# Performance work log

Hardware: AMD Instinct MI355X
Metric: run time of the kernel (lower is better)

The kernel has to match this reference:

```python
import jax, jax.numpy as jnp
import numpy as np

B = 131072
HIDDEN = 256


def setup_inputs() -> dict:
    key = jax.random.key(0)
    ks = jax.random.split(key, 9)
    x = jax.random.uniform(ks[0], (B, 2), dtype=jnp.float32)
    # torch nn.Linear weights are [out_features, in_features]; kaiming-uniform-ish scale
    def w(k, out_f, in_f):
        bound = 1.0 / np.sqrt(in_f)
        return jax.random.uniform(k, (out_f, in_f), jnp.float32, -bound, bound)
    W0 = w(ks[1], HIDDEN, 2)
    W1 = w(ks[2], HIDDEN, HIDDEN)
    W2 = w(ks[3], HIDDEN, HIDDEN)
    W3 = w(ks[4], HIDDEN, HIDDEN)
    W4 = w(ks[5], HIDDEN, HIDDEN)
    W5 = w(ks[6], HIDDEN, HIDDEN)
    W6 = w(ks[7], HIDDEN, HIDDEN)
    W7 = w(ks[8], 3, HIDDEN)
    return {"x": x, "W0": W0, "W1": W1, "W2": W2, "W3": W3,
            "W4": W4, "W5": W5, "W6": W6, "W7": W7}


def reference(x, W0, W1, W2, W3, W4, W5, W6, W7):
    # 8 bias-free Linear layers: ReLU after layers 0..6, Sigmoid after layer 7.
    h = x
    for W in (W0, W1, W2, W3, W4, W5, W6):
        h = jax.nn.relu(h @ W.T)
    return jax.nn.sigmoid(h @ W7.T)  # [B, 3]
```

## Files before the change

kernel.cpp:

```cpp
#include <hip/hip_runtime.h>
#include <hip/hip_bf16.h>


#define HID 256
#define BM 128
#define NBLK 1024
#define HPITCH 264

typedef __attribute__((ext_vector_type(8))) short bf16x8;
typedef __attribute__((ext_vector_type(8))) unsigned short u16x8;
typedef __attribute__((ext_vector_type(4))) unsigned short u16x4;
typedef __attribute__((ext_vector_type(4))) float f32x4;
typedef __attribute__((ext_vector_type(16))) float f32x16;

__device__ __forceinline__ unsigned cvt_pk_bf16(float lo, float hi) {
    unsigned r;
    asm("v_cvt_pk_bf16_f32 %0, %1, %2" : "=v"(r) : "v"(lo), "v"(hi));
    return r;
}

struct WPtrs { const float* w[6]; const float* w7; };

__global__ void pack_w_kernel(WPtrs wp, unsigned short* __restrict__ Wp) {
    int tid = blockIdx.x * 256 + threadIdx.x;
    if (tid < 49152) {
        int l  = tid & 63;
        int ft = (tid >> 6) & 1;
        int kk = (tid >> 7) & 15;
        int fw = (tid >> 11) & 3;
        int L  = tid >> 13;
        int n  = 64 * fw + 32 * ft + (l & 31);
        int k0 = 16 * kk + 8 * (l >> 5);
        const float* src = wp.w[L] + n * HID + k0;
        u16x8 v;
#pragma unroll
        for (int j = 0; j < 8; ++j) {
            union { float f; unsigned u; } c; c.f = src[j];
            unsigned r = c.u + 0x7fffu + ((c.u >> 16) & 1u);
            v[j] = (unsigned short)(r >> 16);
        }
        *(u16x8*)(Wp + (size_t)tid * 8) = v;
    } else if (tid < 49664) {
        int t  = tid - 49152;
        int l  = t & 63;
        int kk = t >> 6;
        int n  = l & 15;
        int k0 = 32 * kk + 8 * (l >> 4);
        u16x8 v;
#pragma unroll
        for (int j = 0; j < 8; ++j) {
            unsigned short s = 0;
            if (n < 3) {
                union { float f; unsigned u; } c; c.f = wp.w7[n * HID + k0 + j];
                s = (unsigned short)((c.u + 0x7fffu + ((c.u >> 16) & 1u)) >> 16);
            }
            v[j] = s;
        }
        *(u16x8*)(Wp + 393216 + (size_t)t * 8) = v;
    }
}

__launch_bounds__(512, 1)
__global__ void mlp_fused_kernel(const float* __restrict__ x,
                                 const float* __restrict__ W0,
                                 const unsigned short* __restrict__ Wp,
                                 float* __restrict__ out) {
    __shared__ __align__(16) unsigned short Hs[2][BM][HPITCH];
    __shared__ __align__(16) float Ps[4][BM][4];
    __shared__ float xsf[2 * BM];

    const int tid = threadIdx.x;
    const int l   = tid & 63;
    const int w   = tid >> 6;
    const int fw  = w & 3;
    const int rb  = (w >> 2) * 64;
    const long r0 = (long)blockIdx.x * BM;

    const unsigned short* wbl = Wp + (size_t)fw * 16384 + (size_t)l * 8;

    bf16x8 wb[3][2];
    wb[0][0] = *(const bf16x8*)(wbl);
    wb[0][1] = *(const bf16x8*)(wbl + 512);
    wb[1][0] = *(const bf16x8*)(wbl + 1024);
    wb[1][1] = *(const bf16x8*)(wbl + 1536);

    const unsigned short* w7b = Wp + 393216 + (size_t)l * 8;
    bf16x8 w7f0 = *(const bf16x8*)(w7b + (2 * fw) * 512);
    bf16x8 w7f1 = *(const bf16x8*)(w7b + (2 * fw + 1) * 512);

    if (tid < 2 * BM) xsf[tid] = x[r0 * 2 + tid];
    const int fp = (tid & 127) * 2;
    const int q  = tid >> 7;
    f32x4 w0v = *(const f32x4*)(W0 + 2 * fp);
    __syncthreads();

#pragma unroll
    for (int i = 0; i < 32; ++i) {
        int m = 32 * q + i;
        float x0 = xsf[2 * m], x1 = xsf[2 * m + 1];
        float ha = fmaf(x0, w0v[0], x1 * w0v[1]);
        float hb = fmaf(x0, w0v[2], x1 * w0v[3]);
        *(unsigned*)(&Hs[0][m][fp]) = cvt_pk_bf16(fmaxf(0.f, ha), fmaxf(0.f, hb));
    }
    __syncthreads();

    const int c  = l & 31;
    const int hi = l >> 5;
#pragma unroll
    for (int L = 0; L < 6; ++L) {
        const int rp = L & 1, wp2 = rp ^ 1;
        f32x16 acc[2][2];
#pragma unroll
        for (int ft = 0; ft < 2; ++ft)
#pragma unroll
            for (int mt = 0; mt < 2; ++mt)
#pragma unroll
                for (int j = 0; j < 16; ++j) acc[ft][mt][j] = 0.f;

#pragma unroll
        for (int kk = 0; kk < 16; ++kk) {
            const int g   = 16 * L + kk;
            const int cur = g % 3;
            const int pre = (g + 2) % 3;
            if (g + 2 < 96) {
                const int gl = (g + 2) >> 4, gk = (g + 2) & 15;
                wb[pre][0] = *(const bf16x8*)(wbl + gl * 65536 + gk * 1024);
                wb[pre][1] = *(const bf16x8*)(wbl + gl * 65536 + gk * 1024 + 512);
            }
            bf16x8 a0 = *(const bf16x8*)(&Hs[rp][rb + c][16 * kk + 8 * hi]);
            bf16x8 a1 = *(const bf16x8*)(&Hs[rp][rb + 32 + c][16 * kk + 8 * hi]);
            acc[0][0] = __builtin_amdgcn_mfma_f32_32x32x16_bf16(wb[cur][0], a0, acc[0][0], 0, 0, 0);
            acc[0][1] = __builtin_amdgcn_mfma_f32_32x32x16_bf16(wb[cur][0], a1, acc[0][1], 0, 0, 0);
            acc[1][0] = __builtin_amdgcn_mfma_f32_32x32x16_bf16(wb[cur][1], a0, acc[1][0], 0, 0, 0);
            acc[1][1] = __builtin_amdgcn_mfma_f32_32x32x16_bf16(wb[cur][1], a1, acc[1][1], 0, 0, 0);
        }
#pragma unroll
        for (int ft = 0; ft < 2; ++ft)
#pragma unroll
            for (int mt = 0; mt < 2; ++mt) {
                f32x16 v = acc[ft][mt];
#pragma unroll
                for (int g2 = 0; g2 < 4; ++g2) {
                    union { unsigned u[2]; u16x4 s; } pk;
                    pk.u[0] = cvt_pk_bf16(fmaxf(0.f, v[4 * g2]),     fmaxf(0.f, v[4 * g2 + 1]));
                    pk.u[1] = cvt_pk_bf16(fmaxf(0.f, v[4 * g2 + 2]), fmaxf(0.f, v[4 * g2 + 3]));
                    *(u16x4*)(&Hs[wp2][rb + 32 * mt + c][64 * fw + 32 * ft + 8 * g2 + 4 * hi]) = pk.s;
                }
            }
        __syncthreads();
    }

    const int lr = l & 15, lg = l >> 4;
    f32x4 acc7[4];
#pragma unroll
    for (int mt = 0; mt < 4; ++mt) acc7[mt] = (f32x4){0.f, 0.f, 0.f, 0.f};
#pragma unroll
    for (int mt = 0; mt < 4; ++mt) {
        bf16x8 a = *(const bf16x8*)(&Hs[0][rb + 16 * mt + lr][32 * (2 * fw) + 8 * lg]);
        acc7[mt] = __builtin_amdgcn_mfma_f32_16x16x32_bf16(w7f0, a, acc7[mt], 0, 0, 0);
        bf16x8 b = *(const bf16x8*)(&Hs[0][rb + 16 * mt + lr][32 * (2 * fw + 1) + 8 * lg]);
        acc7[mt] = __builtin_amdgcn_mfma_f32_16x16x32_bf16(w7f1, b, acc7[mt], 0, 0, 0);
    }
    if (lg == 0) {
#pragma unroll
        for (int mt = 0; mt < 4; ++mt)
            *(f32x4*)(&Ps[fw][rb + 16 * mt + lr][0]) = acc7[mt];
    }
    __syncthreads();
    if (tid < 3 * BM) {
        int row = tid / 3, o = tid - 3 * row;
        float s = Ps[0][row][o] + Ps[1][row][o] + Ps[2][row][o] + Ps[3][row][o];
        out[r0 * 3 + tid] = 1.f / (1.f + __expf(-s));
    }
}

extern "C" void kernel_launch(void* const* d_in, const int* in_sizes, int n_in,
                              void* d_out, int out_size, void* d_ws, size_t ws_size,
                              hipStream_t stream) {
    const float* x  = (const float*)d_in[0];
    const float* W0 = (const float*)d_in[1];
    WPtrs wp;
    for (int i = 0; i < 6; ++i) wp.w[i] = (const float*)d_in[2 + i];
    wp.w7 = (const float*)d_in[8];
    float* out = (float*)d_out;
    unsigned short* Wp = (unsigned short*)d_ws;

    pack_w_kernel<<<194, 256, 0, stream>>>(wp, Wp);
    mlp_fused_kernel<<<NBLK, 512, 0, stream>>>(x, W0, Wp, out);
}
```

Before: 170.7 us.

## Halve row tile and single-buffer activations to raise blocks per CU

Rows per block drop from 128 to 64 and the grid doubles. The activation buffer goes from double to single buffered, with an extra barrier between the MFMA reads and the ReLU writeback, and the launch bounds ask for 4 blocks per CU. Each wave now owns one 32-row strip with two accumulators instead of four, which cuts register and LDS use so more blocks can overlap weight loads and MFMA work. In exchange every weight fragment is reused half as often, so global/L2 weight traffic doubles, and the added barrier per layer serializes compute and writeback inside a block.

```diff
diff --git a/kernel.cpp b/kernel.cpp
--- a/kernel.cpp
+++ b/kernel.cpp
@@ -3,8 +3,8 @@
 
 
 #define HID 256
-#define BM 128
-#define NBLK 1024
+#define BM 64
+#define NBLK 2048
 #define HPITCH 264
 
 typedef __attribute__((ext_vector_type(8))) short bf16x8;
@@ -60,33 +60,29 @@
     }
 }
 
-__launch_bounds__(512, 1)
+__launch_bounds__(512, 4)
 __global__ void mlp_fused_kernel(const float* __restrict__ x,
                                  const float* __restrict__ W0,
                                  const unsigned short* __restrict__ Wp,
                                  float* __restrict__ out) {
-    __shared__ __align__(16) unsigned short Hs[2][BM][HPITCH];
+    __shared__ __align__(16) unsigned short Hs[BM][HPITCH];
     __shared__ __align__(16) float Ps[4][BM][4];
     __shared__ float xsf[2 * BM];
 
     const int tid = threadIdx.x;
     const int l   = tid & 63;
     const int w   = tid >> 6;
-    const int fw  = w & 3;
-    const int rb  = (w >> 2) * 64;
+    const int fs  = w & 3;
+    const int rg  = w >> 2;
     const long r0 = (long)blockIdx.x * BM;
 
-    const unsigned short* wbl = Wp + (size_t)fw * 16384 + (size_t)l * 8;
+    const unsigned short* wbl = Wp + (size_t)fs * 16384 + (size_t)l * 8;
 
     bf16x8 wb[3][2];
     wb[0][0] = *(const bf16x8*)(wbl);
     wb[0][1] = *(const bf16x8*)(wbl + 512);
     wb[1][0] = *(const bf16x8*)(wbl + 1024);
     wb[1][1] = *(const bf16x8*)(wbl + 1536);
-
-    const unsigned short* w7b = Wp + 393216 + (size_t)l * 8;
-    bf16x8 w7f0 = *(const bf16x8*)(w7b + (2 * fw) * 512);
-    bf16x8 w7f1 = *(const bf16x8*)(w7b + (2 * fw + 1) * 512);
 
     if (tid < 2 * BM) xsf[tid] = x[r0 * 2 + tid];
     const int fp = (tid & 127) * 2;
@@ -95,12 +91,12 @@
     __syncthreads();
 
 #pragma unroll
-    for (int i = 0; i < 32; ++i) {
-        int m = 32 * q + i;
+    for (int i = 0; i < 16; ++i) {
+        int m = 16 * q + i;
         float x0 = xsf[2 * m], x1 = xsf[2 * m + 1];
         float ha = fmaf(x0, w0v[0], x1 * w0v[1]);
         float hb = fmaf(x0, w0v[2], x1 * w0v[3]);
-        *(unsigned*)(&Hs[0][m][fp]) = cvt_pk_bf16(fmaxf(0.f, ha), fmaxf(0.f, hb));
+        *(unsigned*)(&Hs[m][fp]) = cvt_pk_bf16(fmaxf(0.f, ha), fmaxf(0.f, hb));
     }
     __syncthreads();
 
@@ -108,14 +104,11 @@
     const int hi = l >> 5;
 #pragma unroll
     for (int L = 0; L < 6; ++L) {
-        const int rp = L & 1, wp2 = rp ^ 1;
-        f32x16 acc[2][2];
+        f32x16 acc[2];
 #pragma unroll
         for (int ft = 0; ft < 2; ++ft)
 #pragma unroll
-            for (int mt = 0; mt < 2; ++mt)
-#pragma unroll
-                for (int j = 0; j < 16; ++j) acc[ft][mt][j] = 0.f;
+            for (int j = 0; j < 16; ++j) acc[ft][j] = 0.f;
 
 #pragma unroll
         for (int kk = 0; kk < 16; ++kk) {
@@ -127,44 +120,43 @@
                 wb[pre][0] = *(const bf16x8*)(wbl + gl * 65536 + gk * 1024);
                 wb[pre][1] = *(const bf16x8*)(wbl + gl * 65536 + gk * 1024 + 512);
             }
-            bf16x8 a0 = *(const bf16x8*)(&Hs[rp][rb + c][16 * kk + 8 * hi]);
-            bf16x8 a1 = *(const bf16x8*)(&Hs[rp][rb + 32 + c][16 * kk + 8 * hi]);
-            acc[0][0] = __builtin_amdgcn_mfma_f32_32x32x16_bf16(wb[cur][0], a0, acc[0][0], 0, 0, 0);
-            acc[0][1] = __builtin_amdgcn_mfma_f32_32x32x16_bf16(wb[cur][0], a1, acc[0][1], 0, 0, 0);
-            acc[1][0] = __builtin_amdgcn_mfma_f32_32x32x16_bf16(wb[cur][1], a0, acc[1][0], 0, 0, 0);
-            acc[1][1] = __builtin_amdgcn_mfma_f32_32x32x16_bf16(wb[cur][1], a1, acc[1][1], 0, 0, 0);
+            bf16x8 a0 = *(const bf16x8*)(&Hs[32 * rg + c][16 * kk + 8 * hi]);
+            acc[0] = __builtin_amdgcn_mfma_f32_32x32x16_bf16(wb[cur][0], a0, acc[0], 0, 0, 0);
+            acc[1] = __builtin_amdgcn_mfma_f32_32x32x16_bf16(wb[cur][1], a0, acc[1], 0, 0, 0);
         }
+        __syncthreads();
 #pragma unroll
-        for (int ft = 0; ft < 2; ++ft)
+        for (int ft = 0; ft < 2; ++ft) {
+            f32x16 v = acc[ft];
 #pragma unroll
-            for (int mt = 0; mt < 2; ++mt) {
-                f32x16 v = acc[ft][mt];
-#pragma unroll
-                for (int g2 = 0; g2 < 4; ++g2) {
-                    union { unsigned u[2]; u16x4 s; } pk;
-                    pk.u[0] = cvt_pk_bf16(fmaxf(0.f, v[4 * g2]),     fmaxf(0.f, v[4 * g2 + 1]));
-                    pk.u[1] = cvt_pk_bf16(fmaxf(0.f, v[4 * g2 + 2]), fmaxf(0.f, v[4 * g2 + 3]));
-                    *(u16x4*)(&Hs[wp2][rb + 32 * mt + c][64 * fw + 32 * ft + 8 * g2 + 4 * hi]) = pk.s;
-                }
+            for (int g2 = 0; g2 < 4; ++g2) {
+                union { unsigned u[2]; u16x4 s; } pk;
+                pk.u[0] = cvt_pk_bf16(fmaxf(0.f, v[4 * g2]),     fmaxf(0.f, v[4 * g2 + 1]));
+                pk.u[1] = cvt_pk_bf16(fmaxf(0.f, v[4 * g2 + 2]), fmaxf(0.f, v[4 * g2 + 3]));
+                *(u16x4*)(&Hs[32 * rg + c][64 * fs + 32 * ft + 8 * g2 + 4 * hi]) = pk.s;
             }
+        }
         __syncthreads();
     }
 
     const int lr = l & 15, lg = l >> 4;
-    f32x4 acc7[4];
+    const unsigned short* w7b = Wp + 393216 + (size_t)l * 8;
+    bf16x8 w7f0 = *(const bf16x8*)(w7b + (2 * fs) * 512);
+    bf16x8 w7f1 = *(const bf16x8*)(w7b + (2 * fs + 1) * 512);
+    f32x4 acc7[2];
 #pragma unroll
-    for (int mt = 0; mt < 4; ++mt) acc7[mt] = (f32x4){0.f, 0.f, 0.f, 0.f};
+    for (int mt = 0; mt < 2; ++mt) acc7[mt] = (f32x4){0.f, 0.f, 0.f, 0.f};
 #pragma unroll
-    for (int mt = 0; mt < 4; ++mt) {
-        bf16x8 a = *(const bf16x8*)(&Hs[0][rb + 16 * mt + lr][32 * (2 * fw) + 8 * lg]);
+    for (int mt = 0; mt < 2; ++mt) {
+        bf16x8 a = *(const bf16x8*)(&Hs[32 * rg + 16 * mt + lr][32 * (2 * fs) + 8 * lg]);
         acc7[mt] = __builtin_amdgcn_mfma_f32_16x16x32_bf16(w7f0, a, acc7[mt], 0, 0, 0);
-        bf16x8 b = *(const bf16x8*)(&Hs[0][rb + 16 * mt + lr][32 * (2 * fw + 1) + 8 * lg]);
+        bf16x8 b = *(const bf16x8*)(&Hs[32 * rg + 16 * mt + lr][32 * (2 * fs + 1) + 8 * lg]);
         acc7[mt] = __builtin_amdgcn_mfma_f32_16x16x32_bf16(w7f1, b, acc7[mt], 0, 0, 0);
     }
     if (lg == 0) {
 #pragma unroll
-        for (int mt = 0; mt < 4; ++mt)
-            *(f32x4*)(&Ps[fw][rb + 16 * mt + lr][0]) = acc7[mt];
+        for (int mt = 0; mt < 2; ++mt)
+            *(f32x4*)(&Ps[fs][32 * rg + 16 * mt + lr][0]) = acc7[mt];
     }
     __syncthreads();
     if (tid < 3 * BM) {
```

Result: slower. 188.4 us (+10.3%).
